# Optimization experiments

Measured on AMD Instinct MI355X. Metric: run time of the kernel, lower is better.

Reference implementation:

```python
import jax, jax.numpy as jnp
import numpy as np

N = 50000      # atoms
E = 800000     # edges (avg degree 16)
F = 32         # feature channels
NB = 8         # Bessel basis size
RCUT = 20.0    # Angstrom cutoff (covers the 1nm box)
EV2KJ = 96.4853
NM2A = 10.0


def setup_inputs() -> dict:
    key = jax.random.key(0)
    ks = jax.random.split(key, 12)
    return {
        "positions": jax.random.uniform(ks[0], (N, 3), jnp.float32),      # nm
        "masses": jax.random.uniform(ks[1], (N,), jnp.float32),
        "type_embed": jax.random.normal(ks[2], (3, F), jnp.float32),
        "W_rad1": jax.random.normal(ks[3], (NB, F), jnp.float32) * 0.3,
        "b_rad1": jax.random.normal(ks[4], (F,), jnp.float32) * 0.1,
        "W_rad2": jax.random.normal(ks[5], (F, 2 * F), jnp.float32) * 0.3,
        "W_self": jax.random.normal(ks[6], (F, F), jnp.float32) * 0.3,
        "W_out1": jax.random.normal(ks[7], (2 * F, F), jnp.float32) * 0.3,
        "b_out1": jax.random.normal(ks[8], (F,), jnp.float32) * 0.1,
        "W_out2": jax.random.normal(ks[9], (F, 1), jnp.float32) * 0.3,
        "atom_types": jax.random.randint(ks[10], (N,), 0, 3),
        "edge_index": jax.random.randint(ks[11], (2, E), 0, N),
    }


def reference(positions, masses, type_embed, W_rad1, b_rad1, W_rad2,
              W_self, W_out1, b_out1, W_out2, atom_types, edge_index):
    src, dst = edge_index[0], edge_index[1]

    def energy_eV(pos_A):
        rel = pos_A[dst] - pos_A[src]                       # [E,3] gather
        r = jnp.sqrt(jnp.sum(rel * rel, axis=-1) + 1e-12)   # [E]
        rhat = rel / r[:, None]
        # Bessel radial basis with p=6 polynomial cutoff envelope
        x = r / RCUT
        n = jnp.arange(1, NB + 1, dtype=pos_A.dtype)
        basis = jnp.sin(jnp.pi * n[None, :] * x[:, None]) / r[:, None]  # [E,NB]
        p = 6.0
        env = (1.0 - (p + 1) * (p + 2) / 2 * x**p
               + p * (p + 2) * x**(p + 1)
               - p * (p + 1) / 2 * x**(p + 2))
        env = jnp.where(x < 1.0, env, 0.0)
        rw = jax.nn.silu(basis @ W_rad1 + b_rad1) @ W_rad2   # [E,2F]
        rw = rw * env[:, None]
        w0, w1 = rw[:, :F], rw[:, F:]
        h = type_embed[atom_types]                           # [N,F]
        hs = h[src]                                          # [E,F] gather
        m0 = hs * w0                                         # l=0 messages
        m1 = (hs * w1)[:, :, None] * rhat[:, None, :]        # l=1 messages [E,F,3]
        s = jax.ops.segment_sum(m0, dst, num_segments=N)     # scatter-add
        v = jax.ops.segment_sum(m1.reshape(E, F * 3), dst, num_segments=N)
        v = v.reshape(N, F, 3)
        vnorm = jnp.sqrt(jnp.sum(v * v, axis=-1) + 1e-12)    # invariant [N,F]
        feats = jnp.concatenate([h + s @ W_self, vnorm], axis=1)  # [N,2F]
        per_atom = jax.nn.silu(feats @ W_out1 + b_out1) @ W_out2  # [N,1]
        return jnp.sum(per_atom)

    pos_A = positions * NM2A
    e_eV, g = jax.value_and_grad(energy_eV)(pos_A)
    energy = e_eV * EV2KJ                                    # kJ/mol
    forces = -g * (EV2KJ * NM2A)                             # kJ/mol/nm
    # COM drift correction: mass-weighted net-force subtraction
    net = jnp.sum(forces, axis=0, keepdims=True)
    forces = forces - (masses[:, None] / jnp.sum(masses)) * net
    return energy, forces
```

## Files before the change

kernel.cpp:

```cpp
#include <hip/hip_runtime.h>
#include <math.h>

#define FDIM 32
#define NBASIS 8
#define QP 40
#define DS2 34
#define BINW 4096
#define DCAP 4096
#define GSPLIT 8

constexpr float RCUT_C = 20.0f;
constexpr float PI_F = 3.14159265358979323846f;
constexpr float EV2KJ_C = 96.4853f;
constexpr float NM2A_C = 10.0f;

typedef _Float16 f16x8 __attribute__((ext_vector_type(8)));
typedef _Float16 f16x4 __attribute__((ext_vector_type(4)));
typedef float f32x4 __attribute__((ext_vector_type(4)));

__device__ __forceinline__ float sigmoidf_(float z) { return 1.0f / (1.0f + __expf(-z)); }

__device__ __forceinline__ unsigned int pk2_(float a, float b) {
    unsigned short lo = __builtin_bit_cast(unsigned short, (_Float16)a);
    unsigned short hi = __builtin_bit_cast(unsigned short, (_Float16)b);
    return (unsigned int)lo | ((unsigned int)hi << 16);
}
__device__ __forceinline__ float lo16_(unsigned int v) {
    return (float)__builtin_bit_cast(_Float16, (unsigned short)(v & 0xffffu));
}
__device__ __forceinline__ float hi16_(unsigned int v) {
    return (float)__builtin_bit_cast(_Float16, (unsigned short)(v >> 16));
}

__global__ __launch_bounds__(256) void hist_buckets(
    const int* __restrict__ eidx, int* __restrict__ dbcnt, int* __restrict__ sbcnt,
    int E, int dsh, int ssh, int nbd, int nbs)
{
    __shared__ int ld[512];
    __shared__ int ls[64];
    for (int i = threadIdx.x; i < nbd; i += 256) ld[i] = 0;
    for (int i = threadIdx.x; i < nbs; i += 256) ls[i] = 0;
    __syncthreads();
    for (int e = blockIdx.x * 256 + threadIdx.x; e < E; e += gridDim.x * 256) {
        int s = eidx[e];
        int d = eidx[E + e];
        atomicAdd(&ld[d >> dsh], 1);
        atomicAdd(&ls[s >> ssh], 1);
    }
    __syncthreads();
    for (int i = threadIdx.x; i < nbd; i += 256) if (ld[i]) atomicAdd(&dbcnt[i], ld[i]);
    for (int i = threadIdx.x; i < nbs; i += 256) if (ls[i]) atomicAdd(&sbcnt[i], ls[i]);
}

__global__ __launch_bounds__(512) void scan_bases(
    const int* __restrict__ dbcnt, const int* __restrict__ sbcnt,
    int* __restrict__ dbbase, int* __restrict__ sbbase, int nbd, int nbs)
{
    __shared__ int buf[512];
    const int t = threadIdx.x;
    int v = (t < nbd) ? dbcnt[t] : 0;
    buf[t] = v;
    __syncthreads();
    for (int off = 1; off < 512; off <<= 1) {
        int u = (t >= off) ? buf[t - off] : 0;
        __syncthreads();
        buf[t] += u;
        __syncthreads();
    }
    if (t < nbd) dbbase[t] = buf[t] - v;
    if (t == 511) dbbase[nbd] = buf[511];
// ... 54 lines not shown
    __shared__ int c128[128], o128[128];
    __shared__ int sc[64], sbres[64], so[64];
    const int b = blockIdx.x, t = threadIdx.x;
    const int base = dbbase[b];
    const int cnt = dbbase[b + 1] - base;
    const bool dosort = (dsh <= 7);
    const int kmask = (1 << dsh) - 1;

    for (int start = 0; start < cnt; start += DCAP) {
        const int n = min(DCAP, cnt - start);
        if (t < 128) c128[t] = 0;
        if (t < 64) sc[t] = 0;
        __syncthreads();
        for (int i = t; i < n; i += 256) {
            int2 r = order_sd[base + start + i];
            rec[i] = r;
            if (dosort) atomicAdd(&c128[r.y & kmask], 1);
            atomicAdd(&sc[r.x >> ssh], 1);
        }
        __syncthreads();
        int v0 = (t < 128) ? c128[t] : 0;
        __syncthreads();
        for (int off = 1; off < 128; off <<= 1) {
            int u = (t < 128 && t >= off) ? c128[t - off] : 0;
            __syncthreads();
            if (t < 128) c128[t] += u;
            __syncthreads();
        }
        if (t < 128) o128[t] = c128[t] - v0;
        if (t < 64) {
            int c = sc[t];
            sbres[t] = c ? atomicAdd(&sbcur[t], c) : 0;
            so[t] = 0;
        }
        __syncthreads();
        for (int i = t; i < n; i += 256) {
            int2 r = rec[i];
            int p;
            if (dosort) {
                int pos = atomicAdd(&o128[r.y & kmask], 1);
                p = base + start + pos;
                order_sd[p] = r;
            } else {
                p = base + start + i;
            }
            int sb2 = r.x >> ssh;
            int slot = sbres[sb2] + atomicAdd(&so[sb2], 1);
            srcbin[sbbase[sb2] + slot] = make_int2(r.x, p);
        }
        __syncthreads();
    }
}

__global__ __launch_bounds__(64) void pack_wfrag(
    const float* __restrict__ Wr1, const float* __restrict__ Wr2,
    _Float16* __restrict__ wpack)
{
    const int lane = threadIdx.x;
    const int kb = (lane >> 4) * 8, nb = lane & 15;
    _Float16* o = wpack + (size_t)lane * 64;
    #pragma unroll
    for (int t = 0; t < 2; t++)
        #pragma unroll
        for (int j = 0; j < 8; j++) {
            int k = kb + j;
            o[t * 8 + j] = (k < 8) ? (_Float16)Wr1[k * FDIM + t * 16 + nb] : (_Float16)0.0f;
        }
    #pragma unroll
    for (int t = 0; t < 4; t++)
        #pragma unroll
        for (int j = 0; j < 8; j++)
            o[16 + t * 8 + j] = (_Float16)Wr2[(kb + j) * 64 + t * 16 + nb];
    #pragma unroll
    for (int t = 0; t < 2; t++)
        #pragma unroll
        for (int j = 0; j < 8; j++) {
            int k = kb + j;
            o[48 + t * 8 + j] = (k >= 8 && k < 16) ? (_Float16)Wr1[(k - 8) * FDIM + t * 16 + nb]
                                                   : (_Float16)0.0f;
        }
}

__global__ __launch_bounds__(256) void edge_fwd_mfma(
    const float* __restrict__ pos, const int* __restrict__ types,
    const int2* __restrict__ order_sd,
    const _Float16* __restrict__ wpack, const float* __restrict__ br1,
    const float* __restrict__ temb,
    float* __restrict__ s_acc, float* __restrict__ v_acc, int E)
{
    __shared__ __align__(16) _Float16 sR[4][2560];
    __shared__ float sSt[4][32][4];
    __shared__ int sTy[4][32];
    __shared__ int sKey[4][32];
    __shared__ float sTemb[96];

    const int lane = threadIdx.x & 63;
    const int l32 = threadIdx.x & 31;
    const int w = threadIdx.x >> 6;
    const int gbase = blockIdx.x * 128 + w * 32;

    for (int i = threadIdx.x; i < 96; i += 256) sTemb[i] = temb[i];
    __syncthreads();

    const int kb = (lane >> 4) * 8;
    const f16x8* wp = (const f16x8*)(wpack + (size_t)lane * 64);
    f16x8 bz[2] = { wp[0], wp[1] };
    f16x8 bf[4] = { wp[2], wp[3], wp[4], wp[5] };

    if (lane < 32) {
        const int ed = l32;
        const int p = gbase + ed;
        const bool vld = (p < E);
        int2 sd = vld ? order_sd[p] : make_int2(0, 0);
        float rx = (pos[sd.y * 3 + 0] - pos[sd.x * 3 + 0]) * NM2A_C;
        float ry = (pos[sd.y * 3 + 1] - pos[sd.x * 3 + 1]) * NM2A_C;
        float rz = (pos[sd.y * 3 + 2] - pos[sd.x * 3 + 2]) * NM2A_C;
        float r2 = rx * rx + ry * ry + rz * rz + 1e-12f;
        float r = sqrtf(r2);
        float rinv = 1.0f / r;
        float x = r * (1.0f / RCUT_C);
        float x2 = x * x, x4 = x2 * x2, x6 = x4 * x2, x7 = x6 * x, x8 = x6 * x2;
        float env = (x < 1.0f) ? (1.0f - 28.0f * x6 + 48.0f * x7 - 21.0f * x8) : 0.0f;

        float th = PI_F * x, s1, c1;
        __sincosf(th, &s1, &c1);
        float sp = 0.0f, sn = s1;
        _Float16 av[8];
        #pragma unroll
        for (int n = 0; n < NBASIS; n++) {
            av[n] = (_Float16)(sn * rinv);
            float snx = 2.0f * c1 * sn - sp; sp = sn; sn = snx;
        }
        _Float16* dstA = &sR[w][(ed < 16 ? 0 : 640) + (ed & 15) * QP];
        *(f16x8*)&dstA[0] = *(f16x8*)&av[0];
        *(float4*)&dstA[8]  = make_float4(0.f, 0.f, 0.f, 0.f);
        *(float4*)&dstA[16] = make_float4(0.f, 0.f, 0.f, 0.f);
        *(float4*)&dstA[24] = make_float4(0.f, 0.f, 0.f, 0.f);
        sSt[w][ed][0] = env;
        sSt[w][ed][1] = rx * rinv;
        sSt[w][ed][2] = ry * rinv;
        sSt[w][ed][3] = rz * rinv;
        sTy[w][ed] = types[sd.x];
        sKey[w][ed] = vld ? sd.y : -1;
    }

    {
        const int me = lane & 15;
        f16x8 a1a = *(const f16x8*)&sR[w][me * QP + kb];
        f16x8 a1b = *(const f16x8*)&sR[w][640 + me * QP + kb];
        const f32x4 z4 = {0.f, 0.f, 0.f, 0.f};
        f32x4 Dz0a = __builtin_amdgcn_mfma_f32_16x16x32_f16(a1a, bz[0], z4, 0, 0, 0);
        f32x4 Dz1a = __builtin_amdgcn_mfma_f32_16x16x32_f16(a1a, bz[1], z4, 0, 0, 0);
        f32x4 Dz0b = __builtin_amdgcn_mfma_f32_16x16x32_f16(a1b, bz[0], z4, 0, 0, 0);
        f32x4 Dz1b = __builtin_amdgcn_mfma_f32_16x16x32_f16(a1b, bz[1], z4, 0, 0, 0);
        const int f0 = lane & 15, e0 = (lane >> 4) * 4;
        const float bb0 = br1[f0], bb1 = br1[16 + f0];
        #pragma unroll
        for (int t = 0; t < 2; t++) {
            f32x4 Dza = t ? Dz1a : Dz0a;
            f32x4 Dzb = t ? Dz1b : Dz0b;
            float bb = t ? bb1 : bb0;
            #pragma unroll
            for (int r = 0; r < 4; r++) {
                float za = Dza[r] + bb;
                float zb = Dzb[r] + bb;
                sR[w][1280 + (e0 + r) * QP + t * 16 + f0] = (_Float16)(za * sigmoidf_(za));
                sR[w][1920 + (e0 + r) * QP + t * 16 + f0] = (_Float16)(zb * sigmoidf_(zb));
            }
        }
    }

    {
        const int me = lane & 15;
        f16x8 aqa = *(const f16x8*)&sR[w][1280 + me * QP + kb];
        f16x8 aqb = *(const f16x8*)&sR[w][1920 + me * QP + kb];
        const int cb = lane & 15, e0 = (lane >> 4) * 4;
        float hev[2][2][4];
        #pragma unroll
        for (int tl = 0; tl < 2; tl++)
            #pragma unroll
            for (int fp = 0; fp < 2; fp++)
                #pragma unroll
                for (int r = 0; r < 4; r++) {
                    int ed = tl * 16 + e0 + r;
                    hev[tl][fp][r] = sTemb[sTy[w][ed] * 32 + fp * 16 + cb] * sSt[w][ed][0];
                }
        const f32x4 z4 = {0.f, 0.f, 0.f, 0.f};
        unsigned int* DU = (unsigned int*)&sR[w][0];
        #pragma unroll
        for (int fp = 0; fp < 2; fp++) {
            f32x4 a0 = __builtin_amdgcn_mfma_f32_16x16x32_f16(aqa, bf[fp],     z4, 0, 0, 0);
            f32x4 a1 = __builtin_amdgcn_mfma_f32_16x16x32_f16(aqa, bf[fp + 2], z4, 0, 0, 0);
            f32x4 b0 = __builtin_amdgcn_mfma_f32_16x16x32_f16(aqb, bf[fp],     z4, 0, 0, 0);
            f32x4 b1 = __builtin_amdgcn_mfma_f32_16x16x32_f16(aqb, bf[fp + 2], z4, 0, 0, 0);
            #pragma unroll
            for (int r = 0; r < 4; r++) {
                float ha = hev[0][fp][r], hb = hev[1][fp][r];
                DU[(e0 + r) * 32 + fp * 16 + cb]        = pk2_(a0[r] * ha, a1[r] * ha);
                DU[(16 + e0 + r) * 32 + fp * 16 + cb]   = pk2_(b0[r] * hb, b1[r] * hb);
            }
        }
    }

    {
        const unsigned int* DU = (const unsigned int*)&sR[w][0];
        const bool loHalf = (lane < 32);
        const int mmax = min(32, E - gbase);
        int runKey = -1;
        float a0 = 0.f, a1 = 0.f;
        for (int m = 0; m < mmax; m++) {
            int k = sKey[w][m];
            if (k != runKey) {
                if (runKey >= 0) {
                    float* p0 = loHalf ? &s_acc[(size_t)runKey * 32 + l32]
                                       : &v_acc[(size_t)runKey * 96 + l32];
                    float* p1 = loHalf ? &v_acc[(size_t)runKey * 96 + 32 + l32]
                                       : &v_acc[(size_t)runKey * 96 + 64 + l32];
                    unsafeAtomicAdd(p0, a0);
                    unsafeAtomicAdd(p1, a1);
                }
                runKey = k;
                a0 = a1 = 0.f;
            }
            unsigned int qp = DU[m * 32 + l32];
            float lo = lo16_(qp), hi = hi16_(qp);
            float rA = sSt[w][m][1], rY = sSt[w][m][2], rZ = sSt[w][m][3];
            a0 += loHalf ? lo : hi * rA;
            a1 += hi * (loHalf ? rY : rZ);
        }
        if (runKey >= 0) {
            float* p0 = loHalf ? &s_acc[(size_t)runKey * 32 + l32]
                               : &v_acc[(size_t)runKey * 96 + l32];
            float* p1 = loHalf ? &v_acc[(size_t)runKey * 96 + 32 + l32]
                               : &v_acc[(size_t)runKey * 96 + 64 + l32];
            unsafeAtomicAdd(p0, a0);
            unsafeAtomicAdd(p1, a1);
        }
    }
}

__global__ __launch_bounds__(64) void atom_mlp(
    const int* __restrict__ types, const float* __restrict__ temb,
    const float* __restrict__ Wself, const float* __restrict__ Wo1,
    const float* __restrict__ bo1, const float* __restrict__ Wo2,
    const float* __restrict__ s_acc, const float* __restrict__ v_acc,
    float* __restrict__ g_all, float* __restrict__ out, int N)
{
    __shared__ __align__(16) float sWs[FDIM * FDIM];
    __shared__ __align__(16) float sWo1[2 * FDIM * FDIM];
    __shared__ __align__(16) float sb[FDIM], sW2o[FDIM], sTE[96];
    const int t = threadIdx.x;
    for (int i = t; i < FDIM * FDIM; i += 64) sWs[i] = Wself[i];
    for (int i = t; i < 2 * FDIM * FDIM; i += 64) sWo1[i] = Wo1[i];
    if (t < FDIM) { sb[t] = bo1[t]; sW2o[t] = Wo2[t]; }
    for (int i = t; i < 96; i += 64) sTE[i] = temb[i];
    __syncthreads();

    int a = blockIdx.x * 64 + t;
    const bool valid = (a < N);
    if (!valid) a = 0;
    const int ty = types[a];

    float u[32];
    {
        float row[32];
        #pragma unroll
        for (int j = 0; j < 32; j++) row[j] = sTE[ty * FDIM + j];
        {
            float s_[32];
            #pragma unroll
            for (int q = 0; q < 8; q++) {
                float4 v = *(const float4*)&s_acc[(size_t)a * FDIM + q * 4];
                s_[q * 4 + 0] = v.x; s_[q * 4 + 1] = v.y;
                s_[q * 4 + 2] = v.z; s_[q * 4 + 3] = v.w;
            }
            #pragma unroll
            for (int k = 0; k < 32; k++) {
                float sk = s_[k];
// ... 75 lines not shown
        float ar = 0.f;
        #pragma unroll
        for (int q = 0; q < 8; q++) {
            float4 w1 = *(const float4*)&sWo1[j * 32 + q * 4];
            ar += u[q * 4 + 0] * w1.x + u[q * 4 + 1] * w1.y
                + u[q * 4 + 2] * w1.z + u[q * 4 + 3] * w1.w;
        }
        gfr[j] = ar;
    }

    float gs[32];
    #pragma unroll
    for (int j = 0; j < 32; j++) {
        float acc = 0.f;
        #pragma unroll
        for (int q = 0; q < 8; q++) {
            float4 wv = *(const float4*)&sWs[j * 32 + q * 4];
            acc += gfr[q * 4 + 0] * wv.x + gfr[q * 4 + 1] * wv.y
                 + gfr[q * 4 + 2] * wv.z + gfr[q * 4 + 3] * wv.w;
        }
        gs[j] = acc;
    }

    if (valid) {
        #pragma unroll
        for (int q = 0; q < 8; q++) {
            float4 x4 = *(const float4*)&v_acc[(size_t)a * 96 +      q * 4];
            float4 y4 = *(const float4*)&v_acc[(size_t)a * 96 + 32 + q * 4];
            float4 z4 = *(const float4*)&v_acc[(size_t)a * 96 + 64 + q * 4];
            {
                int j = q * 4 + 0;
                *(float4*)&g_all[(size_t)a * 128 + j * 4] =
                    make_float4(gs[j], sc[j] * x4.x, sc[j] * y4.x, sc[j] * z4.x);
            }
            {
                int j = q * 4 + 1;
                *(float4*)&g_all[(size_t)a * 128 + j * 4] =
                    make_float4(gs[j], sc[j] * x4.y, sc[j] * y4.y, sc[j] * z4.y);
            }
            {
                int j = q * 4 + 2;
                *(float4*)&g_all[(size_t)a * 128 + j * 4] =
                    make_float4(gs[j], sc[j] * x4.z, sc[j] * y4.z, sc[j] * z4.z);
            }
            {
                int j = q * 4 + 3;
                *(float4*)&g_all[(size_t)a * 128 + j * 4] =
                    make_float4(gs[j], sc[j] * x4.w, sc[j] * y4.w, sc[j] * z4.w);
            }
        }
    }
}

__global__ __launch_bounds__(256) void edge_bwd_mfma(
    const float* __restrict__ pos, const int* __restrict__ types,
    const int2* __restrict__ order_sd,
    const _Float16* __restrict__ wpack, const float* __restrict__ br1,
    const float* __restrict__ temb,
    const float* __restrict__ g_all,
    float* __restrict__ forces, float4* __restrict__ fbuf, int E)
{
    __shared__ __align__(16) _Float16 sW[4][4352];
    __shared__ int   sTy[4][32];
    __shared__ float sTemb[96];

    const int lane = threadIdx.x & 63;
    const int el = lane & 31;
    const int w = threadIdx.x >> 6;
    const int gbase = blockIdx.x * 128 + w * 32;

    for (int i = threadIdx.x; i < 96; i += 256) sTemb[i] = temb[i];
    __syncthreads();

    const int kb = (lane >> 4) * 8;
    const f16x8* wp = (const f16x8*)(wpack + (size_t)lane * 64);
    f16x8 bz[2] = { wp[0], wp[1] };
    f16x8 bf[4] = { wp[2], wp[3], wp[4], wp[5] };
    f16x8 bt[2] = { wp[6], wp[7] };

    const int p_e = gbase + el;
    const bool valid = (p_e < E);
    int2 sd = valid ? order_sd[p_e] : make_int2(0, 0);
    const int dstI = sd.y;
    const int key = valid ? sd.y : (-2 - el);

    float rinv = 1.f, env = 0.f, denv = 0.f, rhx = 0.f, rhy = 0.f, rhz = 0.f;
    if (lane < 32) {
        float rx = (pos[sd.y * 3 + 0] - pos[sd.x * 3 + 0]) * NM2A_C;
        float ry = (pos[sd.y * 3 + 1] - pos[sd.x * 3 + 1]) * NM2A_C;
        float rz = (pos[sd.y * 3 + 2] - pos[sd.x * 3 + 2]) * NM2A_C;
        float r2 = rx * rx + ry * ry + rz * rz + 1e-12f;
        float r = sqrtf(r2);
        rinv = 1.0f / r;
        float x = r * (1.0f / RCUT_C);
        float x2 = x * x, x4 = x2 * x2, x5 = x4 * x, x6 = x4 * x2, x7 = x6 * x, x8 = x6 * x2;
        env = (x < 1.0f) ? (1.0f - 28.0f * x6 + 48.0f * x7 - 21.0f * x8) : 0.0f;
        denv = (x < 1.0f) ? (-168.0f * x5 + 336.0f * x6 - 168.0f * x7) * (1.0f / RCUT_C) : 0.0f;
        rhx = rx * rinv; rhy = ry * rinv; rhz = rz * rinv;

        float th = PI_F * x, s1, c1;
        __sincosf(th, &s1, &c1);
        float sp = 0.0f, sn = s1, cp = 1.0f, cn = c1;
        _Float16 av[16];
        #pragma unroll
        for (int n = 0; n < NBASIS; n++) {
            float basis = sn * rinv;
            float dbdr = (PI_F * (float)(n + 1) * (1.0f / RCUT_C)) * cn * rinv - basis * rinv;
            av[n] = (_Float16)basis;
            av[8 + n] = (_Float16)dbdr;
            float snx = 2.0f * c1 * sn - sp; sp = sn; sn = snx;
            float cnx = 2.0f * c1 * cn - cp; cp = cn; cn = cnx;
        }
        _Float16* dstA = &sW[w][(el >> 4) * 640 + (el & 15) * QP];
        *(f16x8*)&dstA[0] = *(f16x8*)&av[0];
        *(f16x8*)&dstA[8] = *(f16x8*)&av[8];
        *(float4*)&dstA[16] = make_float4(0.f, 0.f, 0.f, 0.f);
        *(float4*)&dstA[24] = make_float4(0.f, 0.f, 0.f, 0.f);
        sTy[w][el] = types[sd.x];
    }

    const int fg = lane >> 5;
    const float* gb = g_all + (size_t)dstI * 128;
    float4 gg[8];
    #pragma unroll
    for (int i = 0; i < 8; i++) gg[i] = *(const float4*)(gb + (fg * 16 + i) * 4);

    {
        const int me = lane & 15;
        f16x8 a1a = *(const f16x8*)&sW[w][me * QP + kb];
        f16x8 a1b = *(const f16x8*)&sW[w][640 + me * QP + kb];
        const f32x4 z4 = {0.f, 0.f, 0.f, 0.f};
        f32x4 Dz0a = __builtin_amdgcn_mfma_f32_16x16x32_f16(a1a, bz[0], z4, 0, 0, 0);
        f32x4 Dz1a = __builtin_amdgcn_mfma_f32_16x16x32_f16(a1a, bz[1], z4, 0, 0, 0);
        f32x4 Dt0a = __builtin_amdgcn_mfma_f32_16x16x32_f16(a1a, bt[0], z4, 0, 0, 0);
        f32x4 Dt1a = __builtin_amdgcn_mfma_f32_16x16x32_f16(a1a, bt[1], z4, 0, 0, 0);
        f32x4 Dz0b = __builtin_amdgcn_mfma_f32_16x16x32_f16(a1b, bz[0], z4, 0, 0, 0);
        f32x4 Dz1b = __builtin_amdgcn_mfma_f32_16x16x32_f16(a1b, bz[1], z4, 0, 0, 0);
        f32x4 Dt0b = __builtin_amdgcn_mfma_f32_16x16x32_f16(a1b, bt[0], z4, 0, 0, 0);
        f32x4 Dt1b = __builtin_amdgcn_mfma_f32_16x16x32_f16(a1b, bt[1], z4, 0, 0, 0);
        const int f0 = lane & 15, e0 = (lane >> 4) * 4;
        const float bb0 = br1[f0], bb1 = br1[16 + f0];
        #pragma unroll
        for (int tl = 0; tl < 2; tl++) {
            #pragma unroll
            for (int t = 0; t < 2; t++) {
                f32x4 Dz = tl ? (t ? Dz1b : Dz0b) : (t ? Dz1a : Dz0a);
                f32x4 Dt = tl ? (t ? Dt1b : Dt0b) : (t ? Dt1a : Dt0a);
                float bb = t ? bb1 : bb0;
                #pragma unroll
                for (int r = 0; r < 4; r++) {
                    float z = Dz[r] + bb;
                    float sg = sigmoidf_(z);
                    sW[w][1280 + tl * 640 + (e0 + r) * QP + t * 16 + f0] = (_Float16)(z * sg);
                    sW[w][2560 + tl * 640 + (e0 + r) * QP + t * 16 + f0] =
                        (_Float16)((sg * (1.0f + z * (1.0f - sg))) * Dt[r]);
                }
            }
        }
    }

    {
        const int me = lane & 15;
        f16x8 aqa = *(const f16x8*)&sW[w][1280 + me * QP + kb];
        f16x8 aqb = *(const f16x8*)&sW[w][1920 + me * QP + kb];
        f16x8 ata = *(const f16x8*)&sW[w][2560 + me * QP + kb];
        f16x8 atb = *(const f16x8*)&sW[w][3200 + me * QP + kb];
        const int cb = lane & 15, e0 = (lane >> 4) * 4;
        float hsv[2][2][4];
        #pragma unroll
        for (int tl = 0; tl < 2; tl++)
            #pragma unroll
            for (int r = 0; r < 4; r++) {
                int ty = sTy[w][tl * 16 + e0 + r];
                hsv[tl][0][r] = sTemb[ty * 32 + cb];
                hsv[tl][1][r] = sTemb[ty * 32 + 16 + cb];
            }
        const f32x4 z4 = {0.f, 0.f, 0.f, 0.f};
        unsigned int* Du = (unsigned int*)&sW[w][0];
        #pragma unroll
        for (int fp = 0; fp < 2; fp++) {
            f32x4 q0a = __builtin_amdgcn_mfma_f32_16x16x32_f16(aqa, bf[fp],     z4, 0, 0, 0);
            f32x4 q1a = __builtin_amdgcn_mfma_f32_16x16x32_f16(aqa, bf[fp + 2], z4, 0, 0, 0);
            f32x4 q0b = __builtin_amdgcn_mfma_f32_16x16x32_f16(aqb, bf[fp],     z4, 0, 0, 0);
            f32x4 q1b = __builtin_amdgcn_mfma_f32_16x16x32_f16(aqb, bf[fp + 2], z4, 0, 0, 0);
            f32x4 t0a = __builtin_amdgcn_mfma_f32_16x16x32_f16(ata, bf[fp],     z4, 0, 0, 0);
            f32x4 t1a = __builtin_amdgcn_mfma_f32_16x16x32_f16(ata, bf[fp + 2], z4, 0, 0, 0);
            f32x4 t0b = __builtin_amdgcn_mfma_f32_16x16x32_f16(atb, bf[fp],     z4, 0, 0, 0);
            f32x4 t1b = __builtin_amdgcn_mfma_f32_16x16x32_f16(atb, bf[fp + 2], z4, 0, 0, 0);
            const int f = fp * 16 + cb;
            {
                unsigned int pq[4], pt[4];
                #pragma unroll
                for (int r = 0; r < 4; r++) {
                    float h = hsv[0][fp][r];
                    pq[r] = pk2_(q0a[r] * h, q1a[r] * h);
                    pt[r] = pk2_(t0a[r] * h, t1a[r] * h);
                }
                *(uint4*)&Du[(f * DS2 + e0) * 2]     = make_uint4(pq[0], pt[0], pq[1], pt[1]);
                *(uint4*)&Du[(f * DS2 + e0 + 2) * 2] = make_uint4(pq[2], pt[2], pq[3], pt[3]);
            }
            {
                unsigned int pq[4], pt[4];
                #pragma unroll
                for (int r = 0; r < 4; r++) {
                    float h = hsv[1][fp][r];
                    pq[r] = pk2_(q0b[r] * h, q1b[r] * h);
                    pt[r] = pk2_(t0b[r] * h, t1b[r] * h);
                }
                *(uint4*)&Du[(f * DS2 + 16 + e0) * 2]     = make_uint4(pq[0], pt[0], pq[1], pt[1]);
                *(uint4*)&Du[(f * DS2 + 16 + e0 + 2) * 2] = make_uint4(pq[2], pt[2], pq[3], pt[3]);
            }
        }
    }

    {
        const unsigned int* Du = (const unsigned int*)&sW[w][0];
        float Aa = 0.f, Bb = 0.f, Cc = 0.f, Pp = 0.f;
        float Ap = 0.f, Bp = 0.f, Cp = 0.f, Qq = 0.f;
        #pragma unroll
        for (int ff = 0; ff < 16; ff++) {
            const int f = fg * 16 + ff;
            uint2 qt = *(const uint2*)&Du[(f * DS2 + el) * 2];
            float rw0 = lo16_(qt.x), rw1 = hi16_(qt.x);
            float u0 = lo16_(qt.y), u1 = hi16_(qt.y);
            float4 g4 = (ff < 8) ? gg[ff] : *(const float4*)(gb + f * 4);
            Pp += rw0 * g4.x; Qq += u0 * g4.x;
            Aa += rw1 * g4.y; Bb += rw1 * g4.z; Cc += rw1 * g4.w;
            Ap += u1 * g4.y;  Bp += u1 * g4.z;  Cp += u1 * g4.w;
        }
        Pp += __shfl_xor(Pp, 32, 64); Qq += __shfl_xor(Qq, 32, 64);
        Aa += __shfl_xor(Aa, 32, 64); Bb += __shfl_xor(Bb, 32, 64);
        Cc += __shfl_xor(Cc, 32, 64); Ap += __shfl_xor(Ap, 32, 64);
        Bp += __shfl_xor(Bp, 32, 64); Cp += __shfl_xor(Cp, 32, 64);

        if (lane < 32) {
            float Gx = env * Aa, Gy = env * Bb, Gz = env * Cc;
            float genv = Pp + rhx * Aa + rhy * Bb + rhz * Cc;
            float pc = env * (Qq + rhx * Ap + rhy * Bp + rhz * Cp) + genv * denv;
            float dotg = Gx * rhx + Gy * rhy + Gz * rhz;
            float cx = pc * rhx + (Gx - dotg * rhx) * rinv;
            float cy = pc * rhy + (Gy - dotg * rhy) * rinv;
            float cz = pc * rhz + (Gz - dotg * rhz) * rinv;

            const float SC = EV2KJ_C * NM2A_C;
            if (valid) fbuf[p_e] = make_float4(SC * cx, SC * cy, SC * cz, 0.0f);

            int kk = key;
            #pragma unroll
            for (int d = 1; d < 32; d <<= 1) {
                float ux = __shfl_up(cx, d, 32);
                float uy = __shfl_up(cy, d, 32);
                float uz = __shfl_up(cz, d, 32);
                int uk = __shfl_up(kk, d, 32);
                if (el >= d && uk == kk) { cx += ux; cy += uy; cz += uz; }
            }
            int nk = __shfl_down(kk, 1, 32);
            bool leader = (el == 31) || (nk != kk);
            if (valid && leader) {
                unsafeAtomicAdd(&forces[(size_t)dstI * 3 + 0], -SC * cx);
                unsafeAtomicAdd(&forces[(size_t)dstI * 3 + 1], -SC * cy);
                unsafeAtomicAdd(&forces[(size_t)dstI * 3 + 2], -SC * cz);
            }
        }
    }
}

__global__ __launch_bounds__(256) void gather_src(
    float* __restrict__ forces, const int* __restrict__ sbbase,
    const int2* __restrict__ srcbin, const float4* __restrict__ fbuf,
    int ssh, int N)
{
    __shared__ float acc[3072];
    const int wg = blockIdx.x;
    const int b = wg / GSPLIT, part = wg % GSPLIT;
    const int base = sbbase[b];
    const int cnt = sbbase[b + 1] - base;
    const int r0 = base + (int)((long long)cnt * part / GSPLIT);
// ... 67 lines not shown
{
    int i = blockIdx.x * 256 + threadIdx.x;
    if (i < N) {
        float c = masses[i] / accum[3];
        f[i * 3 + 0] -= c * accum[0];
        f[i * 3 + 1] -= c * accum[1];
        f[i * 3 + 2] -= c * accum[2];
    }
}

extern "C" void kernel_launch(void* const* d_in, const int* in_sizes, int n_in,
                              void* d_out, int out_size, void* d_ws, size_t ws_size,
                              hipStream_t stream)
{
    (void)n_in; (void)ws_size;
    const float* pos    = (const float*)d_in[0];
    const float* masses = (const float*)d_in[1];
    const float* temb   = (const float*)d_in[2];
    const float* Wr1    = (const float*)d_in[3];
    const float* br1    = (const float*)d_in[4];
    const float* Wr2    = (const float*)d_in[5];
    const float* Wself  = (const float*)d_in[6];
    const float* Wo1    = (const float*)d_in[7];
    const float* bo1    = (const float*)d_in[8];
    const float* Wo2    = (const float*)d_in[9];
    const int* types    = (const int*)d_in[10];
    const int* eidx     = (const int*)d_in[11];
    const int N = in_sizes[1];
    const int E = in_sizes[11] / 2;

    float* out = (float*)d_out;
    float* forces = out + 1;

    int dsh = 7;  while (((N + (1 << dsh) - 1) >> dsh) > 512) dsh++;
    int nbd = (N + (1 << dsh) - 1) >> dsh;
    int ssh = 10; while (((N + (1 << ssh) - 1) >> ssh) > 64) ssh++;
    int nbs = (N + (1 << ssh) - 1) >> ssh;

    float* ws = (float*)d_ws;
    float* s_acc = ws;
    float* v_acc = s_acc + (size_t)N * FDIM;
    float* g_all = v_acc + (size_t)N * 96;
    float* accum = g_all + (size_t)N * 128;
    int* meta = (int*)(accum + 4);
    int* dbcnt  = meta;
    int* sbcnt  = dbcnt + 512;
    int* dbcur  = sbcnt + 64;
    int* sbcur  = dbcur + 512;
    int* dbbase = sbcur + 64;
    int* sbbase = dbbase + 513;
    int2* order_sd = (int2*)(((uintptr_t)(sbbase + 65) + 15) & ~(uintptr_t)15);
    int2* srcbin   = order_sd + E;
    float4* fbuf   = (float4*)(((uintptr_t)(srcbin + E) + 15) & ~(uintptr_t)15);
    _Float16* wpack = (_Float16*)(fbuf + E);

    hipMemsetAsync(d_out, 0, (size_t)out_size * sizeof(float), stream);
    hipMemsetAsync(s_acc, 0, (size_t)N * 128 * sizeof(float), stream);
    hipMemsetAsync(meta, 0, 1152 * sizeof(int), stream);
    hipMemsetAsync(accum, 0, 4 * sizeof(float), stream);

    hist_buckets<<<512, 256, 0, stream>>>(eidx, dbcnt, sbcnt, E, dsh, ssh, nbd, nbs);
    scan_bases<<<1, 512, 0, stream>>>(dbcnt, sbcnt, dbbase, sbbase, nbd, nbs);
    int nBin = (E + BINW - 1) / BINW;
    bin_dst<<<nBin, 256, 0, stream>>>(eidx, dbbase, dbcur, order_sd, E, dsh, nbd);
    sort_bucket<<<nbd, 256, 0, stream>>>(order_sd, dbbase, sbcur, sbbase, srcbin, dsh, ssh);
    pack_wfrag<<<1, 64, 0, stream>>>(Wr1, Wr2, wpack);

    int nAtomBlocks = (N + 63) / 64;
    int nFwdBlocks = (E + 127) / 128;
    int nBwdBlocks = (E + 127) / 128;
    edge_fwd_mfma<<<nFwdBlocks, 256, 0, stream>>>(pos, types, order_sd,
                                                  wpack, br1, temb,
                                                  s_acc, v_acc, E);
    atom_mlp<<<nAtomBlocks, 64, 0, stream>>>(types, temb, Wself, Wo1, bo1, Wo2,
                                             s_acc, v_acc, g_all, out, N);
    edge_bwd_mfma<<<nBwdBlocks, 256, 0, stream>>>(pos, types, order_sd,
                                                  wpack, br1, temb,
                                                  g_all, forces, fbuf, E);
    gather_src<<<nbs * GSPLIT, 256, 0, stream>>>(forces, sbbase, srcbin, fbuf, ssh, N);
    reduce_net<<<64, 256, 0, stream>>>(forces, masses, accum, N);
    correct_forces<<<(N + 255) / 256, 256, 0, stream>>>(forces, masses, accum, N);
}
```

Measured before the change: 366.1 us.

## Replace per-edge radial MLP with precomputed interpolated lookup table

Precomputes the radial network output (and its radial derivative) at 2048 sample points of r in a new build_rtab kernel, then the forward and backward edge kernels linearly interpolate from this table instead of computing the Bessel basis and running two MFMA matmuls per edge. This removes the per-edge tensor-core work and the sigmoid evaluations in exchange for 512 bytes of table reads per edge, which will mostly hit in cache. Linear interpolation adds approximation error relative to the exact MLP, and the derivative is interpolated separately rather than taken as the slope of the interpolant. The forward path now stores results as fp32 in LDS, while the backward path still packs them to fp16.

After: 498.3 us. 1.36x slower.

```diff
diff --git a/kernel.cpp b/kernel.cpp
--- a/kernel.cpp
+++ b/kernel.cpp
@@ -3,19 +3,15 @@
 
 #define FDIM 32
 #define NBASIS 8
-#define QP 40
-#define DS2 34
+#define TBL 2048
 #define BINW 4096
 #define DCAP 4096
 #define GSPLIT 8
 
 constexpr float RCUT_C = 20.0f;
-constexpr float PI_F = 3.14159265358979323846f;
 constexpr float EV2KJ_C = 96.4853f;
 constexpr float NM2A_C = 10.0f;
 
-typedef _Float16 f16x8 __attribute__((ext_vector_type(8)));
-typedef _Float16 f16x4 __attribute__((ext_vector_type(4)));
 typedef float f32x4 __attribute__((ext_vector_type(4)));
 
 __device__ __forceinline__ float sigmoidf_(float z) { return 1.0f / (1.0f + __expf(-z)); }
@@ -176,46 +172,64 @@
     }
 }
 
-__global__ __launch_bounds__(64) void pack_wfrag(
-    const float* __restrict__ Wr1, const float* __restrict__ Wr2,
-    _Float16* __restrict__ wpack)
-{
-    const int lane = threadIdx.x;
-    const int kb = (lane >> 4) * 8, nb = lane & 15;
-    _Float16* o = wpack + (size_t)lane * 64;
-    #pragma unroll
-    for (int t = 0; t < 2; t++)
-        #pragma unroll
-        for (int j = 0; j < 8; j++) {
-            int k = kb + j;
-            o[t * 8 + j] = (k < 8) ? (_Float16)Wr1[k * FDIM + t * 16 + nb] : (_Float16)0.0f;
-        }
-    #pragma unroll
-    for (int t = 0; t < 4; t++)
-        #pragma unroll
-        for (int j = 0; j < 8; j++)
-            o[16 + t * 8 + j] = (_Float16)Wr2[(kb + j) * 64 + t * 16 + nb];
-    #pragma unroll
-    for (int t = 0; t < 2; t++)
-        #pragma unroll
-        for (int j = 0; j < 8; j++) {
-            int k = kb + j;
-            o[48 + t * 8 + j] = (k >= 8 && k < 16) ? (_Float16)Wr1[(k - 8) * FDIM + t * 16 + nb]
-                                                   : (_Float16)0.0f;
-        }
-}
-
-__global__ __launch_bounds__(256) void edge_fwd_mfma(
+__global__ __launch_bounds__(64) void build_rtab(
+    const float* __restrict__ Wr1, const float* __restrict__ br1,
+    const float* __restrict__ Wr2, float* __restrict__ rtab)
+{
+    __shared__ float sil[32], tfv[32];
+    const int i = blockIdx.x;
+    const int t = threadIdx.x;
+    const double x = (double)i / (double)(TBL - 1);
+    const double r = x * (double)RCUT_C;
+    float bas[NBASIS], dbs[NBASIS];
+    #pragma unroll
+    for (int n = 0; n < NBASIS; n++) {
+        double pn = M_PI * (double)(n + 1);
+        if (i == 0) {
+            bas[n] = (float)(pn / (double)RCUT_C);
+            dbs[n] = 0.0f;
+        } else {
+            double a = pn * x;
+            double s = sin(a), c = cos(a);
+            bas[n] = (float)(s / r);
+            dbs[n] = (float)((pn / (double)RCUT_C) * c / r - s / (r * r));
+        }
+    }
+    if (t < 32) {
+        float z = br1[t], dz = 0.0f;
+        #pragma unroll
+        for (int k = 0; k < NBASIS; k++) {
+            z  += bas[k] * Wr1[k * FDIM + t];
+            dz += dbs[k] * Wr1[k * FDIM + t];
+        }
+        float sg = sigmoidf_(z);
+        sil[t] = z * sg;
+        tfv[t] = (sg * (1.0f + z * (1.0f - sg))) * dz;
+    }
+    __syncthreads();
+    float q = 0.0f, tv = 0.0f;
+    #pragma unroll
+    for (int j = 0; j < 32; j++) {
+        float w2 = Wr2[j * 64 + t];
+        q  += sil[j] * w2;
+        tv += tfv[j] * w2;
+    }
+    rtab[(size_t)i * 128 + t]      = q;
+    rtab[(size_t)i * 128 + 64 + t] = tv;
+}
+
+__global__ __launch_bounds__(256) void edge_fwd_tab(
     const float* __restrict__ pos, const int* __restrict__ types,
-    const int2* __restrict__ order_sd,
-    const _Float16* __restrict__ wpack, const float* __restrict__ br1,
+    const int2* __restrict__ order_sd, const float* __restrict__ rtab,
     const float* __restrict__ temb,
     float* __restrict__ s_acc, float* __restrict__ v_acc, int E)
 {
-    __shared__ __align__(16) _Float16 sR[4][2560];
+    __shared__ float sDf[4][64 * 33];
     __shared__ float sSt[4][32][4];
     __shared__ int sTy[4][32];
     __shared__ int sKey[4][32];
+    __shared__ int sIx[4][32];
+    __shared__ float sFr[4][32];
     __shared__ float sTemb[96];
 
     const int lane = threadIdx.x & 63;
@@ -226,14 +240,9 @@
     for (int i = threadIdx.x; i < 96; i += 256) sTemb[i] = temb[i];
     __syncthreads();
 
-    const int kb = (lane >> 4) * 8;
-    const f16x8* wp = (const f16x8*)(wpack + (size_t)lane * 64);
-    f16x8 bz[2] = { wp[0], wp[1] };
-    f16x8 bf[4] = { wp[2], wp[3], wp[4], wp[5] };
-
     if (lane < 32) {
-        const int ed = l32;
-        const int p = gbase + ed;
+        const int m = l32;
+        const int p = gbase + m;
         const bool vld = (p < E);
         int2 sd = vld ? order_sd[p] : make_int2(0, 0);
         float rx = (pos[sd.y * 3 + 0] - pos[sd.x * 3 + 0]) * NM2A_C;
@@ -245,89 +254,43 @@
         float x = r * (1.0f / RCUT_C);
         float x2 = x * x, x4 = x2 * x2, x6 = x4 * x2, x7 = x6 * x, x8 = x6 * x2;
         float env = (x < 1.0f) ? (1.0f - 28.0f * x6 + 48.0f * x7 - 21.0f * x8) : 0.0f;
-
-        float th = PI_F * x, s1, c1;
-        __sincosf(th, &s1, &c1);
-        float sp = 0.0f, sn = s1;
-        _Float16 av[8];
-        #pragma unroll
-        for (int n = 0; n < NBASIS; n++) {
-            av[n] = (_Float16)(sn * rinv);
-            float snx = 2.0f * c1 * sn - sp; sp = sn; sn = snx;
-        }
-        _Float16* dstA = &sR[w][(ed < 16 ? 0 : 640) + (ed & 15) * QP];
-        *(f16x8*)&dstA[0] = *(f16x8*)&av[0];
-        *(float4*)&dstA[8]  = make_float4(0.f, 0.f, 0.f, 0.f);
-        *(float4*)&dstA[16] = make_float4(0.f, 0.f, 0.f, 0.f);
-        *(float4*)&dstA[24] = make_float4(0.f, 0.f, 0.f, 0.f);
-        sSt[w][ed][0] = env;
-        sSt[w][ed][1] = rx * rinv;
-        sSt[w][ed][2] = ry * rinv;
-        sSt[w][ed][3] = rz * rinv;
-        sTy[w][ed] = types[sd.x];
-        sKey[w][ed] = vld ? sd.y : -1;
+        float xs = x * (float)(TBL - 1);
+        int ti = min((int)xs, TBL - 2);
+        sIx[w][m] = ti;
+        sFr[w][m] = xs - (float)ti;
+        sSt[w][m][0] = env;
+        sSt[w][m][1] = rx * rinv;
+        sSt[w][m][2] = ry * rinv;
+        sSt[w][m][3] = rz * rinv;
+        sTy[w][m] = types[sd.x];
+        sKey[w][m] = vld ? sd.y : -1;
     }
 
     {
-        const int me = lane & 15;
-        f16x8 a1a = *(const f16x8*)&sR[w][me * QP + kb];
-        f16x8 a1b = *(const f16x8*)&sR[w][640 + me * QP + kb];
-        const f32x4 z4 = {0.f, 0.f, 0.f, 0.f};
-        f32x4 Dz0a = __builtin_amdgcn_mfma_f32_16x16x32_f16(a1a, bz[0], z4, 0, 0, 0);
-        f32x4 Dz1a = __builtin_amdgcn_mfma_f32_16x16x32_f16(a1a, bz[1], z4, 0, 0, 0);
-        f32x4 Dz0b = __builtin_amdgcn_mfma_f32_16x16x32_f16(a1b, bz[0], z4, 0, 0, 0);
-        f32x4 Dz1b = __builtin_amdgcn_mfma_f32_16x16x32_f16(a1b, bz[1], z4, 0, 0, 0);
-        const int f0 = lane & 15, e0 = (lane >> 4) * 4;
-        const float bb0 = br1[f0], bb1 = br1[16 + f0];
-        #pragma unroll
-        for (int t = 0; t < 2; t++) {
-            f32x4 Dza = t ? Dz1a : Dz0a;
-            f32x4 Dzb = t ? Dz1b : Dz0b;
-            float bb = t ? bb1 : bb0;
+        const int m = lane >> 1, h = lane & 1;
+        const int ti = sIx[w][m];
+        const float fr = sFr[w][m];
+        const float env = sSt[w][m][0];
+        const int ty = sTy[w][m];
+        const float* r0 = rtab + (size_t)ti * 128 + h * 32;
+        const float* r1 = r0 + 128;
+        float* Dc = &sDf[w][0];
+        const int cb = h * 32;
+        #pragma unroll
+        for (int c4 = 0; c4 < 8; c4++) {
+            f32x4 a = *(const f32x4*)(r0 + c4 * 4);
+            f32x4 b = *(const f32x4*)(r1 + c4 * 4);
             #pragma unroll
-            for (int r = 0; r < 4; r++) {
-                float za = Dza[r] + bb;
-                float zb = Dzb[r] + bb;
-                sR[w][1280 + (e0 + r) * QP + t * 16 + f0] = (_Float16)(za * sigmoidf_(za));
-                sR[w][1920 + (e0 + r) * QP + t * 16 + f0] = (_Float16)(zb * sigmoidf_(zb));
+            for (int j = 0; j < 4; j++) {
+                int c = c4 * 4 + j;
+                float v = (a[j] + fr * (b[j] - a[j])) * env * sTemb[ty * 32 + c];
+                Dc[(cb + c) * 33 + m] = v;
             }
         }
     }
 
     {
-        const int me = lane & 15;
-        f16x8 aqa = *(const f16x8*)&sR[w][1280 + me * QP + kb];
-        f16x8 aqb = *(const f16x8*)&sR[w][1920 + me * QP + kb];
-        const int cb = lane & 15, e0 = (lane >> 4) * 4;
-        float hev[2][2][4];
-        #pragma unroll
-        for (int tl = 0; tl < 2; tl++)
-            #pragma unroll
-            for (int fp = 0; fp < 2; fp++)
-                #pragma unroll
-                for (int r = 0; r < 4; r++) {
-                    int ed = tl * 16 + e0 + r;
-                    hev[tl][fp][r] = sTemb[sTy[w][ed] * 32 + fp * 16 + cb] * sSt[w][ed][0];
-                }
-        const f32x4 z4 = {0.f, 0.f, 0.f, 0.f};
-        unsigned int* DU = (unsigned int*)&sR[w][0];
-        #pragma unroll
-        for (int fp = 0; fp < 2; fp++) {
-            f32x4 a0 = __builtin_amdgcn_mfma_f32_16x16x32_f16(aqa, bf[fp],     z4, 0, 0, 0);
-            f32x4 a1 = __builtin_amdgcn_mfma_f32_16x16x32_f16(aqa, bf[fp + 2], z4, 0, 0, 0);
-            f32x4 b0 = __builtin_amdgcn_mfma_f32_16x16x32_f16(aqb, bf[fp],     z4, 0, 0, 0);
-            f32x4 b1 = __builtin_amdgcn_mfma_f32_16x16x32_f16(aqb, bf[fp + 2], z4, 0, 0, 0);
-            #pragma unroll
-            for (int r = 0; r < 4; r++) {
-                float ha = hev[0][fp][r], hb = hev[1][fp][r];
-                DU[(e0 + r) * 32 + fp * 16 + cb]        = pk2_(a0[r] * ha, a1[r] * ha);
-                DU[(16 + e0 + r) * 32 + fp * 16 + cb]   = pk2_(b0[r] * hb, b1[r] * hb);
-            }
-        }
-    }
-
-    {
-        const unsigned int* DU = (const unsigned int*)&sR[w][0];
+        const float* Dc = &sDf[w][0];
         const bool loHalf = (lane < 32);
         const int mmax = min(32, E - gbase);
         int runKey = -1;
@@ -346,8 +309,8 @@
                 runKey = k;
                 a0 = a1 = 0.f;
             }
-            unsigned int qp = DU[m * 32 + l32];
-            float lo = lo16_(qp), hi = hi16_(qp);
+            float hi = Dc[(32 + l32) * 33 + m];
+            float lo = Dc[l32 * 33 + m];
             float rA = sSt[w][m][1], rY = sSt[w][m][2], rZ = sSt[w][m][3];
             a0 += loHalf ? lo : hi * rA;
             a1 += hi * (loHalf ? rY : rZ);
@@ -529,31 +492,27 @@
     }
 }
 
-__global__ __launch_bounds__(256) void edge_bwd_mfma(
+__global__ __launch_bounds__(256) void edge_bwd_tab(
     const float* __restrict__ pos, const int* __restrict__ types,
-    const int2* __restrict__ order_sd,
-    const _Float16* __restrict__ wpack, const float* __restrict__ br1,
-    const float* __restrict__ temb,
-    const float* __restrict__ g_all,
+    const int2* __restrict__ order_sd, const float* __restrict__ rtab,
+    const float* __restrict__ temb, const float* __restrict__ g_all,
     float* __restrict__ forces, float4* __restrict__ fbuf, int E)
 {
-    __shared__ __align__(16) _Float16 sW[4][4352];
-    __shared__ int   sTy[4][32];
+    __shared__ unsigned int sDq[4][32 * 33];
+    __shared__ unsigned int sDt[4][32 * 33];
+    __shared__ int sTy[4][32];
+    __shared__ int sIx[4][32];
+    __shared__ float sFr[4][32];
     __shared__ float sTemb[96];
 
     const int lane = threadIdx.x & 63;
     const int el = lane & 31;
+    const int fg = lane >> 5;
     const int w = threadIdx.x >> 6;
     const int gbase = blockIdx.x * 128 + w * 32;
 
     for (int i = threadIdx.x; i < 96; i += 256) sTemb[i] = temb[i];
     __syncthreads();
-
-    const int kb = (lane >> 4) * 8;
-    const f16x8* wp = (const f16x8*)(wpack + (size_t)lane * 64);
-    f16x8 bz[2] = { wp[0], wp[1] };
-    f16x8 bf[4] = { wp[2], wp[3], wp[4], wp[5] };
-    f16x8 bt[2] = { wp[6], wp[7] };
 
     const int p_e = gbase + el;
     const bool valid = (p_e < E);
@@ -574,132 +533,53 @@
         env = (x < 1.0f) ? (1.0f - 28.0f * x6 + 48.0f * x7 - 21.0f * x8) : 0.0f;
         denv = (x < 1.0f) ? (-168.0f * x5 + 336.0f * x6 - 168.0f * x7) * (1.0f / RCUT_C) : 0.0f;
         rhx = rx * rinv; rhy = ry * rinv; rhz = rz * rinv;
-
-        float th = PI_F * x, s1, c1;
-        __sincosf(th, &s1, &c1);
-        float sp = 0.0f, sn = s1, cp = 1.0f, cn = c1;
-        _Float16 av[16];
-        #pragma unroll
-        for (int n = 0; n < NBASIS; n++) {
-            float basis = sn * rinv;
-            float dbdr = (PI_F * (float)(n + 1) * (1.0f / RCUT_C)) * cn * rinv - basis * rinv;
-            av[n] = (_Float16)basis;
-            av[8 + n] = (_Float16)dbdr;
-            float snx = 2.0f * c1 * sn - sp; sp = sn; sn = snx;
-            float cnx = 2.0f * c1 * cn - cp; cp = cn; cn = cnx;
-        }
-        _Float16* dstA = &sW[w][(el >> 4) * 640 + (el & 15) * QP];
-        *(f16x8*)&dstA[0] = *(f16x8*)&av[0];
-        *(f16x8*)&dstA[8] = *(f16x8*)&av[8];
-        *(float4*)&dstA[16] = make_float4(0.f, 0.f, 0.f, 0.f);
-        *(float4*)&dstA[24] = make_float4(0.f, 0.f, 0.f, 0.f);
+        float xs = x * (float)(TBL - 1);
+        int ti = min((int)xs, TBL - 2);
+        sIx[w][el] = ti;
+        sFr[w][el] = xs - (float)ti;
         sTy[w][el] = types[sd.x];
     }
 
-    const int fg = lane >> 5;
     const float* gb = g_all + (size_t)dstI * 128;
     float4 gg[8];
     #pragma unroll
     for (int i = 0; i < 8; i++) gg[i] = *(const float4*)(gb + (fg * 16 + i) * 4);
 
     {
-        const int me = lane & 15;
-        f16x8 a1a = *(const f16x8*)&sW[w][me * QP + kb];
-        f16x8 a1b = *(const f16x8*)&sW[w][640 + me * QP + kb];
-        const f32x4 z4 = {0.f, 0.f, 0.f, 0.f};
-        f32x4 Dz0a = __builtin_amdgcn_mfma_f32_16x16x32_f16(a1a, bz[0], z4, 0, 0, 0);
-        f32x4 Dz1a = __builtin_amdgcn_mfma_f32_16x16x32_f16(a1a, bz[1], z4, 0, 0, 0);
-        f32x4 Dt0a = __builtin_amdgcn_mfma_f32_16x16x32_f16(a1a, bt[0], z4, 0, 0, 0);
-        f32x4 Dt1a = __builtin_amdgcn_mfma_f32_16x16x32_f16(a1a, bt[1], z4, 0, 0, 0);
-        f32x4 Dz0b = __builtin_amdgcn_mfma_f32_16x16x32_f16(a1b, bz[0], z4, 0, 0, 0);
-        f32x4 Dz1b = __builtin_amdgcn_mfma_f32_16x16x32_f16(a1b, bz[1], z4, 0, 0, 0);
-        f32x4 Dt0b = __builtin_amdgcn_mfma_f32_16x16x32_f16(a1b, bt[0], z4, 0, 0, 0);
-        f32x4 Dt1b = __builtin_amdgcn_mfma_f32_16x16x32_f16(a1b, bt[1], z4, 0, 0, 0);
-        const int f0 = lane & 15, e0 = (lane >> 4) * 4;
-        const float bb0 = br1[f0], bb1 = br1[16 + f0];
-        #pragma unroll
-        for (int tl = 0; tl < 2; tl++) {
+        const int m = lane >> 1, h = lane & 1;
+        const int ti = sIx[w][m];
+        const float fr = sFr[w][m];
+        const int ty = sTy[w][m];
+        const float* r0 = rtab + (size_t)ti * 128 + h * 64;
+        const float* r1 = r0 + 128;
+        unsigned int* plane = h ? &sDt[w][0] : &sDq[w][0];
+        #pragma unroll
+        for (int c4 = 0; c4 < 8; c4++) {
+            f32x4 alo = *(const f32x4*)(r0 + c4 * 4);
+            f32x4 blo = *(const f32x4*)(r1 + c4 * 4);
+            f32x4 ahi = *(const f32x4*)(r0 + 32 + c4 * 4);
+            f32x4 bhi = *(const f32x4*)(r1 + 32 + c4 * 4);
             #pragma unroll
-            for (int t = 0; t < 2; t++) {
-                f32x4 Dz = tl ? (t ? Dz1b : Dz0b) : (t ? Dz1a : Dz0a);
-                f32x4 Dt = tl ? (t ? Dt1b : Dt0b) : (t ? Dt1a : Dt0a);
-                float bb = t ? bb1 : bb0;
-                #pragma unroll
-                for (int r = 0; r < 4; r++) {
-                    float z = Dz[r] + bb;
-                    float sg = sigmoidf_(z);
-                    sW[w][1280 + tl * 640 + (e0 + r) * QP + t * 16 + f0] = (_Float16)(z * sg);
-                    sW[w][2560 + tl * 640 + (e0 + r) * QP + t * 16 + f0] =
-                        (_Float16)((sg * (1.0f + z * (1.0f - sg))) * Dt[r]);
-                }
+            for (int j = 0; j < 4; j++) {
+                int c = c4 * 4 + j;
+                float hs = sTemb[ty * 32 + c];
+                float lo = (alo[j] + fr * (blo[j] - alo[j])) * hs;
+                float hi = (ahi[j] + fr * (bhi[j] - ahi[j])) * hs;
+                plane[c * 33 + m] = pk2_(lo, hi);
             }
         }
     }
 
     {
-        const int me = lane & 15;
-        f16x8 aqa = *(const f16x8*)&sW[w][1280 + me * QP + kb];
-        f16x8 aqb = *(const f16x8*)&sW[w][1920 + me * QP + kb];
-        f16x8 ata = *(const f16x8*)&sW[w][2560 + me * QP + kb];
-        f16x8 atb = *(const f16x8*)&sW[w][3200 + me * QP + kb];
-        const int cb = lane & 15, e0 = (lane >> 4) * 4;
-        float hsv[2][2][4];
-        #pragma unroll
-        for (int tl = 0; tl < 2; tl++)
-            #pragma unroll
-            for (int r = 0; r < 4; r++) {
-                int ty = sTy[w][tl * 16 + e0 + r];
-                hsv[tl][0][r] = sTemb[ty * 32 + cb];
-                hsv[tl][1][r] = sTemb[ty * 32 + 16 + cb];
-            }
-        const f32x4 z4 = {0.f, 0.f, 0.f, 0.f};
-        unsigned int* Du = (unsigned int*)&sW[w][0];
-        #pragma unroll
-        for (int fp = 0; fp < 2; fp++) {
-            f32x4 q0a = __builtin_amdgcn_mfma_f32_16x16x32_f16(aqa, bf[fp],     z4, 0, 0, 0);
-            f32x4 q1a = __builtin_amdgcn_mfma_f32_16x16x32_f16(aqa, bf[fp + 2], z4, 0, 0, 0);
-            f32x4 q0b = __builtin_amdgcn_mfma_f32_16x16x32_f16(aqb, bf[fp],     z4, 0, 0, 0);
-            f32x4 q1b = __builtin_amdgcn_mfma_f32_16x16x32_f16(aqb, bf[fp + 2], z4, 0, 0, 0);
-            f32x4 t0a = __builtin_amdgcn_mfma_f32_16x16x32_f16(ata, bf[fp],     z4, 0, 0, 0);
-            f32x4 t1a = __builtin_amdgcn_mfma_f32_16x16x32_f16(ata, bf[fp + 2], z4, 0, 0, 0);
-            f32x4 t0b = __builtin_amdgcn_mfma_f32_16x16x32_f16(atb, bf[fp],     z4, 0, 0, 0);
-            f32x4 t1b = __builtin_amdgcn_mfma_f32_16x16x32_f16(atb, bf[fp + 2], z4, 0, 0, 0);
-            const int f = fp * 16 + cb;
-            {
-                unsigned int pq[4], pt[4];
-                #pragma unroll
-                for (int r = 0; r < 4; r++) {
-                    float h = hsv[0][fp][r];
-                    pq[r] = pk2_(q0a[r] * h, q1a[r] * h);
-                    pt[r] = pk2_(t0a[r] * h, t1a[r] * h);
-                }
-                *(uint4*)&Du[(f * DS2 + e0) * 2]     = make_uint4(pq[0], pt[0], pq[1], pt[1]);
-                *(uint4*)&Du[(f * DS2 + e0 + 2) * 2] = make_uint4(pq[2], pt[2], pq[3], pt[3]);
-            }
-            {
-                unsigned int pq[4], pt[4];
-                #pragma unroll
-                for (int r = 0; r < 4; r++) {
-                    float h = hsv[1][fp][r];
-                    pq[r] = pk2_(q0b[r] * h, q1b[r] * h);
-                    pt[r] = pk2_(t0b[r] * h, t1b[r] * h);
-                }
-                *(uint4*)&Du[(f * DS2 + 16 + e0) * 2]     = make_uint4(pq[0], pt[0], pq[1], pt[1]);
-                *(uint4*)&Du[(f * DS2 + 16 + e0 + 2) * 2] = make_uint4(pq[2], pt[2], pq[3], pt[3]);
-            }
-        }
-    }
-
-    {
-        const unsigned int* Du = (const unsigned int*)&sW[w][0];
         float Aa = 0.f, Bb = 0.f, Cc = 0.f, Pp = 0.f;
         float Ap = 0.f, Bp = 0.f, Cp = 0.f, Qq = 0.f;
         #pragma unroll
         for (int ff = 0; ff < 16; ff++) {
             const int f = fg * 16 + ff;
-            uint2 qt = *(const uint2*)&Du[(f * DS2 + el) * 2];
-            float rw0 = lo16_(qt.x), rw1 = hi16_(qt.x);
-            float u0 = lo16_(qt.y), u1 = hi16_(qt.y);
+            unsigned int qx = sDq[w][f * 33 + el];
+            unsigned int qy = sDt[w][f * 33 + el];
+            float rw0 = lo16_(qx), rw1 = hi16_(qx);
+            float u0 = lo16_(qy), u1 = hi16_(qy);
             float4 g4 = (ff < 8) ? gg[ff] : *(const float4*)(gb + f * 4);
             Pp += rw0 * g4.x; Qq += u0 * g4.x;
             Aa += rw1 * g4.y; Bb += rw1 * g4.z; Cc += rw1 * g4.w;
@@ -873,31 +753,29 @@
     int2* order_sd = (int2*)(((uintptr_t)(sbbase + 65) + 15) & ~(uintptr_t)15);
     int2* srcbin   = order_sd + E;
     float4* fbuf   = (float4*)(((uintptr_t)(srcbin + E) + 15) & ~(uintptr_t)15);
-    _Float16* wpack = (_Float16*)(fbuf + E);
+    float* rtab    = (float*)(fbuf + E);
 
     hipMemsetAsync(d_out, 0, (size_t)out_size * sizeof(float), stream);
     hipMemsetAsync(s_acc, 0, (size_t)N * 128 * sizeof(float), stream);
     hipMemsetAsync(meta, 0, 1152 * sizeof(int), stream);
     hipMemsetAsync(accum, 0, 4 * sizeof(float), stream);
 
+    build_rtab<<<TBL, 64, 0, stream>>>(Wr1, br1, Wr2, rtab);
     hist_buckets<<<512, 256, 0, stream>>>(eidx, dbcnt, sbcnt, E, dsh, ssh, nbd, nbs);
     scan_bases<<<1, 512, 0, stream>>>(dbcnt, sbcnt, dbbase, sbbase, nbd, nbs);
     int nBin = (E + BINW - 1) / BINW;
     bin_dst<<<nBin, 256, 0, stream>>>(eidx, dbbase, dbcur, order_sd, E, dsh, nbd);
     sort_bucket<<<nbd, 256, 0, stream>>>(order_sd, dbbase, sbcur, sbbase, srcbin, dsh, ssh);
-    pack_wfrag<<<1, 64, 0, stream>>>(Wr1, Wr2, wpack);
 
     int nAtomBlocks = (N + 63) / 64;
     int nFwdBlocks = (E + 127) / 128;
     int nBwdBlocks = (E + 127) / 128;
-    edge_fwd_mfma<<<nFwdBlocks, 256, 0, stream>>>(pos, types, order_sd,
-                                                  wpack, br1, temb,
-                                                  s_acc, v_acc, E);
+    edge_fwd_tab<<<nFwdBlocks, 256, 0, stream>>>(pos, types, order_sd, rtab, temb,
+                                                 s_acc, v_acc, E);
     atom_mlp<<<nAtomBlocks, 64, 0, stream>>>(types, temb, Wself, Wo1, bo1, Wo2,
                                              s_acc, v_acc, g_all, out, N);
-    edge_bwd_mfma<<<nBwdBlocks, 256, 0, stream>>>(pos, types, order_sd,
-                                                  wpack, br1, temb,
-                                                  g_all, forces, fbuf, E);
+    edge_bwd_tab<<<nBwdBlocks, 256, 0, stream>>>(pos, types, order_sd, rtab, temb,
+                                                 g_all, forces, fbuf, E);
     gather_src<<<nbs * GSPLIT, 256, 0, stream>>>(forces, sbbase, srcbin, fbuf, ssh, N);
     reduce_net<<<64, 256, 0, stream>>>(forces, masses, accum, N);
     correct_forces<<<(N + 255) / 256, 256, 0, stream>>>(forces, masses, accum, N);
```
